# Optimization experiments

Measured on AMD Instinct MI355X. Metric: run time of the kernel, lower is better.

The kernel has to match this reference:

```python
import jax, jax.numpy as jnp
import numpy as np

N_HEADS = 16
N_EMBD = 1024
HEAD_SIZE = N_EMBD // N_HEADS
B, T = 4, 2048
EPS = 1e-5


def _layernorm(x, g, b):
    mu = jnp.mean(x, axis=-1, keepdims=True)
    var = jnp.mean((x - mu) ** 2, axis=-1, keepdims=True)
    return (x - mu) * jax.lax.rsqrt(var + EPS) * g + b


def setup_inputs() -> dict:
    key = jax.random.key(0)
    ks = jax.random.split(key, 12)
    s_in = 1.0 / np.sqrt(N_EMBD)
    s_ff = 1.0 / np.sqrt(4 * N_EMBD)
    return {
        "x": jax.random.normal(ks[0], (B, T, N_EMBD), jnp.float32),
        "Wq": jax.random.normal(ks[1], (N_HEADS, N_EMBD, HEAD_SIZE), jnp.float32) * s_in,
        "Wk": jax.random.normal(ks[2], (N_HEADS, N_EMBD, HEAD_SIZE), jnp.float32) * s_in,
        "Wv": jax.random.normal(ks[3], (N_HEADS, N_EMBD, HEAD_SIZE), jnp.float32) * s_in,
        "Wproj": jax.random.normal(ks[4], (N_EMBD, N_EMBD), jnp.float32) * s_in,
        "bproj": jnp.zeros((N_EMBD,), jnp.float32),
        "ln1_g": jnp.ones((N_EMBD,), jnp.float32),
        "ln1_b": jnp.zeros((N_EMBD,), jnp.float32),
        "ln2_g": jnp.ones((N_EMBD,), jnp.float32),
        "ln2_b": jnp.zeros((N_EMBD,), jnp.float32),
        "W1": jax.random.normal(ks[5], (N_EMBD, 4 * N_EMBD), jnp.float32) * s_in,
        "b1": jnp.zeros((4 * N_EMBD,), jnp.float32),
        "W2": jax.random.normal(ks[6], (4 * N_EMBD, N_EMBD), jnp.float32) * s_ff,
        "b2": jnp.zeros((N_EMBD,), jnp.float32),
    }


def reference(x, Wq, Wk, Wv, Wproj, bproj, ln1_g, ln1_b, ln2_g, ln2_b, W1, b1, W2, b2):
    Bx, Tx, C = x.shape
    # --- self-attention on ln1(x) ---
    h = _layernorm(x, ln1_g, ln1_b)
    q = jnp.einsum('btc,hcd->bhtd', h, Wq)
    k = jnp.einsum('btc,hcd->bhtd', h, Wk)
    v = jnp.einsum('btc,hcd->bhtd', h, Wv)
    # NOTE: original scales by C**-0.5 where C = n_embd (full dim), not head_size
    scores = jnp.einsum('bhtd,bhsd->bhts', q, k) * (C ** -0.5)
    causal = jnp.tril(jnp.ones((Tx, Tx), dtype=bool))
    scores = jnp.where(causal, scores, -jnp.inf)
    wei = jax.nn.softmax(scores, axis=-1)
    attn = jnp.einsum('bhts,bhsd->bhtd', wei, v)  # [B,H,T,hs]
    attn = attn.transpose(0, 2, 1, 3).reshape(Bx, Tx, -1)  # concat heads -> [B,T,C]
    x = x + attn @ Wproj + bproj
    # --- feed-forward on ln2(x) ---
    h2 = _layernorm(x, ln2_g, ln2_b)
    ff = jax.nn.relu(h2 @ W1 + b1) @ W2 + b2
    return x + ff
```

## Files before the change

kernel.cpp:

```cpp
#include <hip/hip_runtime.h>
#include <math.h>

typedef short bf16x8 __attribute__((ext_vector_type(8)));
typedef float f32x4 __attribute__((ext_vector_type(4)));
typedef unsigned short u16;

__device__ __forceinline__ u16 f2bf(float f) {
    union { float f; unsigned u; } v; v.f = f;
    unsigned r = v.u + 0x7fffu + ((v.u >> 16) & 1u);
    return (u16)(r >> 16);
}

__device__ __forceinline__ void gload_lds16(const void* g, void* l) {
    __builtin_amdgcn_global_load_lds((const __attribute__((address_space(1))) void*)g,
                                     (__attribute__((address_space(3))) void*)l, 16, 0, 0);
}

__global__ __launch_bounds__(256)
void transpose_cvt(const float* __restrict__ in, u16* __restrict__ out, int R, int C)
{
    __shared__ float tile[64][65];
    const size_t slab = (size_t)blockIdx.z * R * C;
    const float* ip = in + slab;
    u16* op = out + slab;
    const int r0 = blockIdx.y * 64, c0 = blockIdx.x * 64;
    const int t = threadIdx.x;
    const int tr = t >> 6, tc = t & 63;
    #pragma unroll
    for (int i = 0; i < 16; ++i)
        tile[tr + i*4][tc] = ip[(size_t)(r0 + tr + i*4)*C + c0 + tc];
    __syncthreads();
    #pragma unroll
    for (int i = 0; i < 16; ++i)
        op[(size_t)(c0 + tr + i*4)*R + r0 + tc] = f2bf(tile[tc][tr + i*4]);
}

__global__ __launch_bounds__(256)
void ln_kernel(const float* __restrict__ x, const float* __restrict__ g,
               const float* __restrict__ b, u16* __restrict__ out)
{
    const int row = blockIdx.x;
    const int t = threadIdx.x;
    const float4 v = ((const float4*)(x + (size_t)row*1024))[t];
    float s = v.x + v.y + v.z + v.w;
    float ss = v.x*v.x + v.y*v.y + v.z*v.z + v.w*v.w;
    #pragma unroll
    for (int m = 1; m < 64; m <<= 1) {
        s  += __shfl_xor(s, m);
        ss += __shfl_xor(ss, m);
    }
    __shared__ float red[8];
    const int wave = t >> 6;
    if ((t & 63) == 0) { red[wave] = s; red[4 + wave] = ss; }
    __syncthreads();
    s  = red[0] + red[1] + red[2] + red[3];
    ss = red[4] + red[5] + red[6] + red[7];
    const float mu = s * (1.f/1024.f);
    const float rs = rsqrtf(ss * (1.f/1024.f) - mu*mu + 1e-5f);
    const float4 gv = ((const float4*)g)[t];
    const float4 bv = ((const float4*)b)[t];
    ushort4 ov;
    ov.x = f2bf((v.x - mu)*rs*gv.x + bv.x);
    ov.y = f2bf((v.y - mu)*rs*gv.y + bv.y);
    ov.z = f2bf((v.z - mu)*rs*gv.z + bv.z);
    ov.w = f2bf((v.w - mu)*rs*gv.w + bv.w);
    ((ushort4*)(out + (size_t)row*1024))[t] = ov;
}

template<int NWG, int BN, int N, int K, int EPI>
__global__ __launch_bounds__(512, 2)
void gemm256_kernel(const u16* __restrict__ A, const u16* __restrict__ BT,
                    float* __restrict__ out_f32, u16* __restrict__ out_bf16,
                    const float* __restrict__ bias, const float* __restrict__ res,
                    u16* __restrict__ qbuf, u16* __restrict__ kbuf, u16* __restrict__ vt)
{
    constexpr int NI  = BN / 128;
    constexpr int WC  = BN / 4;
    constexpr int SIB = BN / 64;
    __shared__ u16 As[2][256*64];
    __shared__ u16 Bs[2][BN*64];

    const int bid = blockIdx.x;
    const int tid = ((bid & 7) * (NWG / 8)) + (bid >> 3);
    const int m0 = (tid & 31) * 256;
    const int n0 = (tid >> 5) * BN;
    const int t = threadIdx.x;
    const int lane = t & 63;
    const int l15 = lane & 15, lg = lane >> 4;
    const int wid = t >> 6;
    const int wm = wid >> 2, wn = wid & 3;
    const int swzf = (l15 & 7) << 4;

    f32x4 acc[2][2][4][NI] = {};
    bf16x8 af[4][2], b0[NI][2], b1[NI][2];

    const int srow = t >> 3;
    const int sg8  = ((t & 7) ^ (srow & 7)) * 8;

    #define STAGE_G(BUF, K0) do { \
        _Pragma("unroll") \
        for (int i = 0; i < 4; ++i) \
            gload_lds16(A + (size_t)(m0 + i*64 + srow)*K + (K0) + sg8, &As[BUF][i*4096 + t*8]); \
        _Pragma("unroll") \
        for (int i = 0; i < SIB; ++i) \
            gload_lds16(BT + (size_t)(n0 + i*64 + srow)*K + (K0) + sg8, &Bs[BUF][i*4096 + t*8]); \
    } while (0)

    #define RD_A(QM) do { \
        _Pragma("unroll") \
        for (int mi = 0; mi < 4; ++mi) \
            _Pragma("unroll") \
            for (int kk = 0; kk < 2; ++kk) \
                af[mi][kk] = *(const bf16x8*)((const char*)&As[cur][0] \
                    + (wm*128 + (QM)*64 + mi*16 + l15)*128 + ((kk*64 + lg*16) ^ swzf)); \
    } while (0)

    #define RD_B(QN, DST) do { \
        _Pragma("unroll") \
        for (int ni = 0; ni < NI; ++ni) \
            _Pragma("unroll") \
            for (int kk = 0; kk < 2; ++kk) \
                DST[ni][kk] = *(const bf16x8*)((const char*)&Bs[cur][0] \
                    + (wn*WC + (QN)*(WC/2) + ni*16 + l15)*128 + ((kk*64 + lg*16) ^ swzf)); \
    } while (0)

    #define MFMAQ(QM, QN, BF) do { \
        _Pragma("unroll") \
        for (int mi = 0; mi < 4; ++mi) \
            _Pragma("unroll") \
            for (int ni = 0; ni < NI; ++ni) \
                _Pragma("unroll") \
                for (int kk = 0; kk < 2; ++kk) \
                    acc[QM][QN][mi][ni] = __builtin_amdgcn_mfma_f32_16x16x32_bf16( \
                        af[mi][kk], BF[ni][kk], acc[QM][QN][mi][ni], 0, 0, 0); \
    } while (0)

    #define PHASE_PRE()  do { __builtin_amdgcn_sched_barrier(0); __builtin_amdgcn_s_barrier(); \
        asm volatile("s_waitcnt lgkmcnt(0)" ::: "memory"); __builtin_amdgcn_sched_barrier(0); \
        __builtin_amdgcn_s_setprio(1); } while (0)
    #define PHASE_POST() do { __builtin_amdgcn_s_setprio(0); __builtin_amdgcn_sched_barrier(0); \
        __builtin_amdgcn_s_barrier(); } while (0)

    STAGE_G(0, 0);
    asm volatile("s_waitcnt vmcnt(0)" ::: "memory");
    __builtin_amdgcn_s_barrier();

    const int NKT = K / 64;
    for (int kt = 0; kt < NKT; ++kt) {
        const int cur = kt & 1;
        RD_A(0); RD_B(0, b0);
        if (kt + 1 < NKT) STAGE_G(cur ^ 1, (kt + 1) * 64);
        PHASE_PRE();  MFMAQ(0, 0, b0);  PHASE_POST();
        RD_B(1, b1);
        PHASE_PRE();  MFMAQ(0, 1, b1);  PHASE_POST();
        RD_A(1);
        PHASE_PRE();  MFMAQ(1, 1, b1);  PHASE_POST();
        asm volatile("s_waitcnt vmcnt(0)" ::: "memory");
        __builtin_amdgcn_s_barrier();
        __builtin_amdgcn_s_setprio(1);
        MFMAQ(1, 0, b0);
        PHASE_POST();
    }
    #undef STAGE_G
    #undef RD_A
    #undef RD_B
    #undef MFMAQ
    #undef PHASE_PRE
    #undef PHASE_POST

    #pragma unroll
    for (int qm = 0; qm < 2; ++qm)
      #pragma unroll
      for (int qn = 0; qn < 2; ++qn)
        #pragma unroll
        for (int mi = 0; mi < 4; ++mi)
          #pragma unroll
          for (int ni = 0; ni < NI; ++ni) {
            const int gc = n0 + wn*WC + qn*(WC/2) + ni*16 + l15;
            #pragma unroll
            for (int j = 0; j < 4; ++j) {
                const int gr = m0 + wm*128 + qm*64 + mi*16 + lg*4 + j;
                float v = acc[qm][qn][mi][ni][j];
                if constexpr (EPI == 0) {
                    u16 bv = f2bf(v);
                    if (gc < 1024) {
                        qbuf[(size_t)gr*1024 + gc] = bv;
                    } else if (gc < 2048) {
                        kbuf[(size_t)gr*1024 + (gc - 1024)] = bv;
                    } else {
                        const int hd = gc - 2048;
                        const int bb = gr >> 11, tt = gr & 2047;
                        vt[(size_t)((bb*16 + (hd >> 6))*64 + (hd & 63))*2048 + tt] = bv;
                    }
                } else if constexpr (EPI == 1) {
                    out_f32[(size_t)gr*N + gc] = v + bias[gc] + res[(size_t)gr*N + gc];
                } else {
                    out_bf16[(size_t)gr*N + gc] = f2bf(fmaxf(v + bias[gc], 0.f));
                }
            }
          }
}

__device__ __forceinline__ void attn_qtile(
    bf16x8 (&qf)[2][2], f32x4 (&o)[2][4], float (&mprev)[2][4], float (&lsum)[2][4],
    const u16* Ksc, const u16* Vsc, u16* pl,
    int key0, int q0, int l15, int lg, int swzf, int swzp)
{
    #pragma unroll
    for (int mi = 0; mi < 2; ++mi) {
        if (key0 > q0 + mi*16 + 15) continue;
        f32x4 s[4] = {};
        #pragma unroll
        for (int n = 0; n < 4; ++n)
            #pragma unroll
            for (int kk = 0; kk < 2; ++kk) {
                const int row = n*16 + l15;
                bf16x8 kf = *(const bf16x8*)((const char*)Ksc
                                + row*128 + ((kk*64 + lg*16) ^ swzf));
                s[n] = __builtin_amdgcn_mfma_f32_16x16x32_bf16(qf[mi][kk], kf, s[n], 0, 0, 0);
            }
        const bool domask = (key0 + 63) > (q0 + mi*16);
        float tm[4] = {-INFINITY, -INFINITY, -INFINITY, -INFINITY};
        #pragma unroll
        for (int n = 0; n < 4; ++n)
            #pragma unroll
            for (int j = 0; j < 4; ++j) {
                float sv = s[n][j] * 0.03125f;
                if (domask && (key0 + n*16 + l15 > q0 + mi*16 + lg*4 + j)) sv = -INFINITY;
                s[n][j] = sv;
                tm[j] = fmaxf(tm[j], sv);
            }
        #pragma unroll
        for (int m = 1; m < 16; m <<= 1)
            #pragma unroll
            for (int j = 0; j < 4; ++j)
                tm[j] = fmaxf(tm[j], __shfl_xor(tm[j], m, 16));
        float alpha[4], rsum[4];
        #pragma unroll
        for (int j = 0; j < 4; ++j) {
            float mn = fmaxf(mprev[mi][j], tm[j]);
            alpha[j] = __expf(mprev[mi][j] - mn);
            mprev[mi][j] = mn;
            rsum[j] = 0.f;
        }
        #pragma unroll
        for (int n = 0; n < 4; ++n)
            #pragma unroll
            for (int j = 0; j < 4; ++j) {
                float pv = __expf(s[n][j] - mprev[mi][j]);
                rsum[j] += pv;
                const int qq = lg*4 + j;
                pl[qq*64 + ((n*16 + l15) ^ ((qq & 7) * 8))] = f2bf(pv);
            }
        #pragma unroll
        for (int m = 1; m < 16; m <<= 1)
            #pragma unroll
            for (int j = 0; j < 4; ++j)
                rsum[j] += __shfl_xor(rsum[j], m, 16);
        #pragma unroll
        for (int j = 0; j < 4; ++j)
            lsum[mi][j] = lsum[mi][j]*alpha[j] + rsum[j];
        #pragma unroll
        for (int dn = 0; dn < 4; ++dn)
            #pragma unroll
            for (int j = 0; j < 4; ++j)
                o[mi][dn][j] *= alpha[j];
        bf16x8 pf[2];
        #pragma unroll
        for (int kk = 0; kk < 2; ++kk)
            pf[kk] = *(const bf16x8*)(pl + l15*64 + ((kk*32 + lg*8) ^ swzp));
        #pragma unroll
        for (int dn = 0; dn < 4; ++dn)
            #pragma unroll
            for (int kk = 0; kk < 2; ++kk) {
                const int row = dn*16 + l15;
                bf16x8 vf = *(const bf16x8*)((const char*)Vsc
                                + row*128 + ((kk*64 + lg*16) ^ swzf));
                o[mi][dn] = __builtin_amdgcn_mfma_f32_16x16x32_bf16(pf[kk], vf, o[mi][dn], 0, 0, 0);
            }
    }
}

__global__ __launch_bounds__(256, 2)
void attn_kernel(const u16* __restrict__ q, const u16* __restrict__ k,
                 const u16* __restrict__ vt, u16* __restrict__ out)
{
    __shared__ u16 Ks[2][4096];
    __shared__ u16 Vs[2][4096];
    __shared__ u16 Plds[4][1024];

    const int bh = blockIdx.x & 63;
    const int pair = blockIdx.x >> 6;
    const int b = bh >> 4, h = bh & 15;
    const int wave = threadIdx.x >> 6, lane = threadIdx.x & 63;
    const int l15 = lane & 15, lg = lane >> 4;
    const int qA = pair, qB = 15 - pair;
    const int q0A = qA*128 + wave*32;
    const int q0B = qB*128 + wave*32;
    const u16* Qp = q + (size_t)b*2048*1024 + h*64;
    const u16* Kp = k + (size_t)b*2048*1024 + h*64;
    const u16* Vp = vt + (size_t)bh*64*2048;
    u16* pl = Plds[wave];

    bf16x8 qfA[2][2], qfB[2][2];
    #pragma unroll
    for (int mi = 0; mi < 2; ++mi)
        #pragma unroll
        for (int kk = 0; kk < 2; ++kk) {
            qfA[mi][kk] = *(const bf16x8*)(Qp + (size_t)(q0A + mi*16 + l15)*1024 + kk*32 + lg*8);
            qfB[mi][kk] = *(const bf16x8*)(Qp + (size_t)(q0B + mi*16 + l15)*1024 + kk*32 + lg*8);
        }

    const int srow0 = wave*8 + (lane >> 3);
    const int scol  = ((lane & 7) ^ (srow0 & 7)) << 3;
    const int swzf  = (l15 & 7) << 4;
    const int swzp  = (l15 & 7) << 3;

    f32x4 oA[2][4] = {}, oB[2][4] = {};
    float mprevA[2][4], lsumA[2][4], mprevB[2][4], lsumB[2][4];
    #pragma unroll
    for (int mi = 0; mi < 2; ++mi)
        #pragma unroll
        for (int j = 0; j < 4; ++j) {
            mprevA[mi][j] = -INFINITY; lsumA[mi][j] = 0.f;
            mprevB[mi][j] = -INFINITY; lsumB[mi][j] = 0.f;
        }

    const int nkt = 32 - 2*pair;

    #define STAGE(buf, key0_) do { \
        gload_lds16(Kp + (size_t)((key0_) + srow0)*1024 + scol,      &Ks[buf][wave*512]); \
        gload_lds16(Kp + (size_t)((key0_) + srow0 + 32)*1024 + scol, &Ks[buf][(4+wave)*512]); \
        gload_lds16(Vp + (size_t)srow0*2048 + (key0_) + scol,        &Vs[buf][wave*512]); \
        gload_lds16(Vp + (size_t)(srow0+32)*2048 + (key0_) + scol,   &Vs[buf][(4+wave)*512]); \
    } while (0)

    STAGE(0, 0);

    for (int kt = 0; kt < nkt; ++kt) {
        const int cur = kt & 1;
        const int key0 = kt * 64;
        if (kt + 1 < nkt) {
            STAGE(cur ^ 1, key0 + 64);
            asm volatile("s_waitcnt vmcnt(4)" ::: "memory");
        } else {
            asm volatile("s_waitcnt vmcnt(0)" ::: "memory");
        }
        __builtin_amdgcn_s_barrier();
        __builtin_amdgcn_sched_barrier(0);

        if (key0 <= q0A + 31)
            attn_qtile(qfA, oA, mprevA, lsumA, &Ks[cur][0], &Vs[cur][0], pl,
                       key0, q0A, l15, lg, swzf, swzp);
        if (key0 <= q0B + 31)
            attn_qtile(qfB, oB, mprevB, lsumB, &Ks[cur][0], &Vs[cur][0], pl,
                       key0, q0B, l15, lg, swzf, swzp);

        __builtin_amdgcn_sched_barrier(0);
        __builtin_amdgcn_s_barrier();
    }
    #undef STAGE

    #pragma unroll
    for (int mi = 0; mi < 2; ++mi)
        #pragma unroll
        for (int dn = 0; dn < 4; ++dn)
            #pragma unroll
            for (int j = 0; j < 4; ++j) {
                float vA = oA[mi][dn][j] / lsumA[mi][j];
                out[(size_t)(b*2048 + q0A + mi*16 + lg*4 + j)*1024 + h*64 + dn*16 + l15] = f2bf(vA);
                float vB = oB[mi][dn][j] / lsumB[mi][j];
                out[(size_t)(b*2048 + q0B + mi*16 + lg*4 + j)*1024 + h*64 + dn*16 + l15] = f2bf(vB);
            }
}

#define MB(x) ((size_t)(x) << 20)

extern "C" void kernel_launch(void* const* d_in, const int* in_sizes, int n_in,
                              void* d_out, int out_size, void* d_ws, size_t ws_size,
                              hipStream_t stream) {
    const float* x      = (const float*)d_in[0];
    const float* Wq     = (const float*)d_in[1];
    const float* Wk     = (const float*)d_in[2];
    const float* Wv     = (const float*)d_in[3];
    const float* Wproj  = (const float*)d_in[4];
    const float* bproj  = (const float*)d_in[5];
    const float* ln1_g  = (const float*)d_in[6];
    const float* ln1_b  = (const float*)d_in[7];
    const float* ln2_g  = (const float*)d_in[8];
    const float* ln2_b  = (const float*)d_in[9];
    const float* W1     = (const float*)d_in[10];
    const float* b1     = (const float*)d_in[11];
    const float* W2     = (const float*)d_in[12];
    const float* b2     = (const float*)d_in[13];
    float* out = (float*)d_out;

    char* ws = (char*)d_ws;
    u16*  h      = (u16*)(ws + MB(0));
    u16*  qbuf   = (u16*)(ws + MB(16));
    u16*  kbuf   = (u16*)(ws + MB(32));
    u16*  vt     = (u16*)(ws + MB(48));
    u16*  attn   = (u16*)(ws + MB(64));
    float* x2    = (float*)(ws + MB(80));
    u16*  BTqkv  = (u16*)(ws + MB(112));
    u16*  BTproj = (u16*)(ws + MB(118));
    u16*  BT1    = (u16*)(ws + MB(120));
    u16*  BT2    = (u16*)(ws + MB(128));
    u16*  ff     = (u16*)(ws + MB(16));
    u16*  h2     = h;

    transpose_cvt<<<dim3(1,16,16),  256, 0, stream>>>(Wq,    BTqkv,             1024, 64);
    transpose_cvt<<<dim3(1,16,16),  256, 0, stream>>>(Wk,    BTqkv + (1<<20),   1024, 64);
    transpose_cvt<<<dim3(1,16,16),  256, 0, stream>>>(Wv,    BTqkv + (2<<20),   1024, 64);
    transpose_cvt<<<dim3(16,16,1),  256, 0, stream>>>(Wproj, BTproj,            1024, 1024);
    transpose_cvt<<<dim3(64,16,1),  256, 0, stream>>>(W1,    BT1,               1024, 4096);
    transpose_cvt<<<dim3(16,64,1),  256, 0, stream>>>(W2,    BT2,               4096, 1024);

    ln_kernel<<<8192, 256, 0, stream>>>(x, ln1_g, ln1_b, h);
    gemm256_kernel<384,256,3072,1024,0><<<384, 512, 0, stream>>>(h, BTqkv, nullptr, nullptr,
        nullptr, nullptr, qbuf, kbuf, vt);
    attn_kernel<<<512, 256, 0, stream>>>(qbuf, kbuf, vt, attn);
    gemm256_kernel<256,128,1024,1024,1><<<256, 512, 0, stream>>>(attn, BTproj, x2, nullptr,
        bproj, x, nullptr, nullptr, nullptr);
    ln_kernel<<<8192, 256, 0, stream>>>(x2, ln2_g, ln2_b, h2);
    gemm256_kernel<512,256,4096,1024,2><<<512, 512, 0, stream>>>(h2, BT1, nullptr, ff,
        b1, nullptr, nullptr, nullptr, nullptr);
    gemm256_kernel<256,128,1024,4096,1><<<256, 512, 0, stream>>>(ff, BT2, out, nullptr,
        b2, x2, nullptr, nullptr, nullptr);
}
```

Measured before the change: 655.8 us.

## Split GEMM tile staging into halves with fine-grained vmcnt waits

```diff
diff --git a/kernel.cpp b/kernel.cpp
--- a/kernel.cpp
+++ b/kernel.cpp
@@ -75,8 +75,7 @@
                     u16* __restrict__ qbuf, u16* __restrict__ kbuf, u16* __restrict__ vt)
 {
     constexpr int NI  = BN / 128;
-    constexpr int WC  = BN / 4;
-    constexpr int SIB = BN / 64;
+    constexpr int NCB = BN / 64;
     __shared__ u16 As[2][256*64];
     __shared__ u16 Bs[2][BN*64];
 
@@ -97,76 +96,111 @@
     const int srow = t >> 3;
     const int sg8  = ((t & 7) ^ (srow & 7)) * 8;
 
-    #define STAGE_G(BUF, K0) do { \
+#define SA_H(BUF, K0, H) do { \
+    _Pragma("unroll") \
+    for (int i = 2*(H); i < 2*(H)+2; ++i) \
+        gload_lds16(A + (size_t)(m0 + i*64 + srow)*K + (K0) + sg8, &As[BUF][i*4096 + t*8]); \
+} while (0)
+#define SB_H(BUF, K0, H) do { \
+    _Pragma("unroll") \
+    for (int i = (NCB/2)*(H); i < (NCB/2)*(H) + NCB/2; ++i) \
+        gload_lds16(BT + (size_t)(n0 + i*64 + srow)*K + (K0) + sg8, &Bs[BUF][i*4096 + t*8]); \
+} while (0)
+#define RD_A(CUR, QM) do { \
+    _Pragma("unroll") \
+    for (int mi = 0; mi < 4; ++mi) \
         _Pragma("unroll") \
-        for (int i = 0; i < 4; ++i) \
-            gload_lds16(A + (size_t)(m0 + i*64 + srow)*K + (K0) + sg8, &As[BUF][i*4096 + t*8]); \
+        for (int kk = 0; kk < 2; ++kk) \
+            af[mi][kk] = *(const bf16x8*)((const char*)&As[CUR][0] \
+                + ((QM)*128 + wm*64 + mi*16 + l15)*128 + ((kk*64 + lg*16) ^ swzf)); \
+} while (0)
+#define RD_B(CUR, QN, DST) do { \
+    _Pragma("unroll") \
+    for (int ni = 0; ni < NI; ++ni) \
         _Pragma("unroll") \
-        for (int i = 0; i < SIB; ++i) \
-            gload_lds16(BT + (size_t)(n0 + i*64 + srow)*K + (K0) + sg8, &Bs[BUF][i*4096 + t*8]); \
-    } while (0)
-
-    #define RD_A(QM) do { \
-        _Pragma("unroll") \
-        for (int mi = 0; mi < 4; ++mi) \
-            _Pragma("unroll") \
-            for (int kk = 0; kk < 2; ++kk) \
-                af[mi][kk] = *(const bf16x8*)((const char*)&As[cur][0] \
-                    + (wm*128 + (QM)*64 + mi*16 + l15)*128 + ((kk*64 + lg*16) ^ swzf)); \
-    } while (0)
-
-    #define RD_B(QN, DST) do { \
+        for (int kk = 0; kk < 2; ++kk) \
+            DST[ni][kk] = *(const bf16x8*)((const char*)&Bs[CUR][0] \
+                + ((QN)*(BN/2) + wn*(BN/8) + ni*16 + l15)*128 + ((kk*64 + lg*16) ^ swzf)); \
+} while (0)
+#define MFMAQ(QM, QN, BF) do { \
+    _Pragma("unroll") \
+    for (int mi = 0; mi < 4; ++mi) \
         _Pragma("unroll") \
         for (int ni = 0; ni < NI; ++ni) \
             _Pragma("unroll") \
             for (int kk = 0; kk < 2; ++kk) \
-                DST[ni][kk] = *(const bf16x8*)((const char*)&Bs[cur][0] \
-                    + (wn*WC + (QN)*(WC/2) + ni*16 + l15)*128 + ((kk*64 + lg*16) ^ swzf)); \
-    } while (0)
-
-    #define MFMAQ(QM, QN, BF) do { \
-        _Pragma("unroll") \
-        for (int mi = 0; mi < 4; ++mi) \
-            _Pragma("unroll") \
-            for (int ni = 0; ni < NI; ++ni) \
-                _Pragma("unroll") \
-                for (int kk = 0; kk < 2; ++kk) \
-                    acc[QM][QN][mi][ni] = __builtin_amdgcn_mfma_f32_16x16x32_bf16( \
-                        af[mi][kk], BF[ni][kk], acc[QM][QN][mi][ni], 0, 0, 0); \
-    } while (0)
-
-    #define PHASE_PRE()  do { __builtin_amdgcn_sched_barrier(0); __builtin_amdgcn_s_barrier(); \
-        asm volatile("s_waitcnt lgkmcnt(0)" ::: "memory"); __builtin_amdgcn_sched_barrier(0); \
-        __builtin_amdgcn_s_setprio(1); } while (0)
-    #define PHASE_POST() do { __builtin_amdgcn_s_setprio(0); __builtin_amdgcn_sched_barrier(0); \
-        __builtin_amdgcn_s_barrier(); } while (0)
-
-    STAGE_G(0, 0);
-    asm volatile("s_waitcnt vmcnt(0)" ::: "memory");
-    __builtin_amdgcn_s_barrier();
+                acc[QM][QN][mi][ni] = __builtin_amdgcn_mfma_f32_16x16x32_bf16( \
+                    af[mi][kk], BF[ni][kk], acc[QM][QN][mi][ni], 0, 0, 0); \
+} while (0)
+#define PH_MFMA(QM, QN, BF) do { \
+    __builtin_amdgcn_sched_barrier(0); \
+    __builtin_amdgcn_s_barrier(); \
+    asm volatile("s_waitcnt lgkmcnt(0)" ::: "memory"); \
+    __builtin_amdgcn_sched_barrier(0); \
+    __builtin_amdgcn_s_setprio(1); \
+    MFMAQ(QM, QN, BF); \
+    __builtin_amdgcn_s_setprio(0); \
+    __builtin_amdgcn_sched_barrier(0); \
+} while (0)
+#define BAR __builtin_amdgcn_s_barrier()
+#define W_B1S do { if constexpr (BN == 256) asm volatile("s_waitcnt vmcnt(6)":::"memory"); \
+                   else                     asm volatile("s_waitcnt vmcnt(5)":::"memory"); } while (0)
+#define W_A1S do { if constexpr (BN == 256) asm volatile("s_waitcnt vmcnt(6)":::"memory"); \
+                   else                     asm volatile("s_waitcnt vmcnt(4)":::"memory"); } while (0)
+#define W_01S do { if constexpr (BN == 256) asm volatile("s_waitcnt vmcnt(4)":::"memory"); \
+                   else                     asm volatile("s_waitcnt vmcnt(3)":::"memory"); } while (0)
+#define W_B1L asm volatile("s_waitcnt vmcnt(2)":::"memory")
+#define W_A1L asm volatile("s_waitcnt vmcnt(0)":::"memory")
+
+    SA_H(0, 0, 0); SB_H(0, 0, 0);
+    SB_H(0, 0, 1);
+    SA_H(0, 0, 1);
+    W_01S; BAR;
 
     const int NKT = K / 64;
-    for (int kt = 0; kt < NKT; ++kt) {
-        const int cur = kt & 1;
-        RD_A(0); RD_B(0, b0);
-        if (kt + 1 < NKT) STAGE_G(cur ^ 1, (kt + 1) * 64);
-        PHASE_PRE();  MFMAQ(0, 0, b0);  PHASE_POST();
-        RD_B(1, b1);
-        PHASE_PRE();  MFMAQ(0, 1, b1);  PHASE_POST();
-        RD_A(1);
-        PHASE_PRE();  MFMAQ(1, 1, b1);  PHASE_POST();
-        asm volatile("s_waitcnt vmcnt(0)" ::: "memory");
-        __builtin_amdgcn_s_barrier();
-        __builtin_amdgcn_s_setprio(1);
-        MFMAQ(1, 0, b0);
-        PHASE_POST();
+    for (int kt = 0; kt < NKT - 1; ++kt) {
+        const int cur = kt & 1, nxt = cur ^ 1;
+        const int k1 = (kt + 1) * 64;
+        RD_A(cur, 0); RD_B(cur, 0, b0);
+        SA_H(nxt, k1, 0); SB_H(nxt, k1, 0);
+        PH_MFMA(0, 0, b0);
+        W_B1S; BAR;
+        RD_B(cur, 1, b1);
+        SB_H(nxt, k1, 1);
+        PH_MFMA(0, 1, b1);
+        W_A1S; BAR;
+        RD_A(cur, 1);
+        SA_H(nxt, k1, 1);
+        PH_MFMA(1, 1, b1);
+        BAR;
+        PH_MFMA(1, 0, b0);
+        W_01S; BAR;
     }
-    #undef STAGE_G
-    #undef RD_A
-    #undef RD_B
-    #undef MFMAQ
-    #undef PHASE_PRE
-    #undef PHASE_POST
+    {
+        const int cur = (NKT - 1) & 1;
+        RD_A(cur, 0); RD_B(cur, 0, b0);
+        PH_MFMA(0, 0, b0);
+        W_B1L; BAR;
+        RD_B(cur, 1, b1);
+        PH_MFMA(0, 1, b1);
+        W_A1L; BAR;
+        RD_A(cur, 1);
+        PH_MFMA(1, 1, b1);
+        BAR;
+        PH_MFMA(1, 0, b0);
+    }
+#undef SA_H
+#undef SB_H
+#undef RD_A
+#undef RD_B
+#undef MFMAQ
+#undef PH_MFMA
+#undef BAR
+#undef W_B1S
+#undef W_A1S
+#undef W_01S
+#undef W_B1L
+#undef W_A1L
 
     #pragma unroll
     for (int qm = 0; qm < 2; ++qm)
@@ -176,10 +210,10 @@
         for (int mi = 0; mi < 4; ++mi)
           #pragma unroll
           for (int ni = 0; ni < NI; ++ni) {
-            const int gc = n0 + wn*WC + qn*(WC/2) + ni*16 + l15;
+            const int gc = n0 + qn*(BN/2) + wn*(BN/8) + ni*16 + l15;
             #pragma unroll
             for (int j = 0; j < 4; ++j) {
-                const int gr = m0 + wm*128 + qm*64 + mi*16 + lg*4 + j;
+                const int gr = m0 + qm*128 + wm*64 + mi*16 + lg*4 + j;
                 float v = acc[qm][qn][mi][ni][j];
                 if constexpr (EPI == 0) {
                     u16 bv = f2bf(v);
```

After: 603.5 us. 1.09x faster.
